# Kernel optimization log

Measured on AMD Instinct MI355X. Metric: run time of the kernel, lower is better.

Reference implementation:

```python
import math
import jax, jax.numpy as jnp
import numpy as np

B, S, D = 2, 2048, 512
H = 8
DH = D // H  # 64
FF = 2048


def _uniform(key, shape, c):
    return jax.random.uniform(key, shape, jnp.float32, -c, c)


def setup_inputs() -> dict:
    key = jax.random.key(0)
    ks = jax.random.split(key, 16)
    x = jax.random.normal(ks[0], (B, S, D), jnp.float32)
    c_qkv = math.sqrt(6 / (D + DH))
    wq = _uniform(ks[1], (H, D, DH), c_qkv)
    wk = _uniform(ks[2], (H, D, DH), c_qkv)
    wv = _uniform(ks[3], (H, D, DH), c_qkv)
    bq = jnp.zeros((H, DH), jnp.float32)
    bk = jnp.zeros((H, DH), jnp.float32)
    bv = jnp.zeros((H, DH), jnp.float32)
    c_o = math.sqrt(6 / (H * DH + D))
    wo = _uniform(ks[4], (H * DH, D), c_o)  # stored as (in, out)
    bo = jnp.zeros((D,), jnp.float32)
    gamma1 = jnp.ones((D,), jnp.float32)
    beta1 = jnp.zeros((D,), jnp.float32)
    c_ff = math.sqrt(6 / (D + FF))
    w1 = _uniform(ks[5], (D, FF), c_ff)
    b1 = jnp.zeros((FF,), jnp.float32)
    w2 = _uniform(ks[6], (FF, D), c_ff)
    b2 = jnp.zeros((D,), jnp.float32)
    gamma2 = jnp.ones((D,), jnp.float32)
    beta2 = jnp.zeros((D,), jnp.float32)
    return dict(x=x, wq=wq, bq=bq, wk=wk, bk=bk, wv=wv, bv=bv, wo=wo, bo=bo,
                gamma1=gamma1, beta1=beta1, w1=w1, b1=b1, w2=w2, b2=b2,
                gamma2=gamma2, beta2=beta2)


def _layernorm(x, gamma, beta):
    # matches torch: (x - mean) / std(unbiased=False), no epsilon in denom
    mean = jnp.mean(x, axis=-1, keepdims=True)
    var = jnp.mean((x - mean) ** 2, axis=-1, keepdims=True)
    return gamma * (x - mean) / jnp.sqrt(var) + beta


def reference(x, wq, bq, wk, bk, wv, bv, wo, bo, gamma1, beta1, w1, b1, w2, b2, gamma2, beta2):
    # multi-head attention: all heads batched in one einsum (same math as the per-head loop)
    q = jnp.einsum('bsd,hde->bhse', x, wq) + bq[None, :, None, :]
    k = jnp.einsum('bsd,hde->bhse', x, wk) + bk[None, :, None, :]
    v = jnp.einsum('bsd,hde->bhse', x, wv) + bv[None, :, None, :]
    scores = jnp.einsum('bhse,bhte->bhst', q, k) / math.sqrt(DH)  # [B,H,S,S]
    attn = jax.nn.softmax(scores, axis=-1)
    y = jnp.einsum('bhst,bhte->bhse', attn, v)  # [B,H,S,DH]
    y = y.transpose(0, 2, 1, 3).reshape(B, S, H * DH)
    y = y @ wo + bo
    # residual + LN (dropout is identity in eval)
    y = _layernorm(y + x, gamma1, beta1)
    # feedforward
    f = jax.nn.relu(y @ w1 + b1) @ w2 + b2
    out = _layernorm(f + y, gamma2, beta2)
    return out
```

## Files before the change

kernel.cpp:

```cpp
#include <hip/hip_runtime.h>

typedef __bf16 bf16;
typedef __attribute__((ext_vector_type(4))) __bf16 bf16x4;
typedef __attribute__((ext_vector_type(8))) __bf16 bf16x8;
typedef __attribute__((ext_vector_type(4))) float f32x4;
typedef __attribute__((ext_vector_type(16))) float f32x16;

#define DEV __device__ __forceinline__

DEV f32x4 mfma16(bf16x8 a, bf16x8 b, f32x4 c) {
  return __builtin_amdgcn_mfma_f32_16x16x32_bf16(a, b, c, 0, 0, 0);
}
DEV f32x16 mfma32(bf16x8 a, bf16x8 b, f32x16 c) {
  return __builtin_amdgcn_mfma_f32_32x32x16_bf16(a, b, c, 0, 0, 0);
}
DEV void gll16(const bf16* g, bf16* l) {
  __builtin_amdgcn_global_load_lds(
      (const __attribute__((address_space(1))) void*)g,
      (__attribute__((address_space(3))) void*)l, 16, 0, 0);
}
DEV unsigned cvtpk(float a, float b) {
  unsigned r;
  asm("v_cvt_pk_bf16_f32 %0, %1, %2" : "=v"(r) : "v"(a), "v"(b));
  return r;
}
DEV void pl32swap(unsigned& x, unsigned& y) {
  asm("v_permlane32_swap_b32 %0, %1" : "+v"(x), "+v"(y));
}

#define QSCALE 0.18033688f

__global__ __launch_bounds__(256) void prep_k(
    const float* __restrict__ x, const float* __restrict__ wq,
    const float* __restrict__ wk, const float* __restrict__ wv,
    const float* __restrict__ wo, const float* __restrict__ w1,
    const float* __restrict__ w2, const float* __restrict__ bq,
    const float* __restrict__ bk, const float* __restrict__ bv,
    bf16* __restrict__ xb, bf16* __restrict__ wqkvT, bf16* __restrict__ woT,
    bf16* __restrict__ w1T, bf16* __restrict__ w2T, float* __restrict__ cb) {
  const int blk = blockIdx.x, tid = threadIdx.x;
  if (blk < 1024) {
    int i = blk * 256 + tid;
    const float4* p = (const float4*)x + (size_t)i * 2;
    float4 a = p[0], b = p[1];
    bf16x8 o;
    o[0] = (bf16)a.x; o[1] = (bf16)a.y; o[2] = (bf16)a.z; o[3] = (bf16)a.w;
    o[4] = (bf16)b.x; o[5] = (bf16)b.y; o[6] = (bf16)b.z; o[7] = (bf16)b.w;
    ((bf16x8*)xb)[i] = o;
    return;
  }
  if (blk == 1792) {
    for (int i = tid; i < 1536; i += 256)
      cb[i] = i < 512 ? bq[i] : (i < 1024 ? bk[i - 512] : bv[i - 1024]);
    return;
  }
  __shared__ float tile[64][65];
  const int t = blk - 1024;
  const float* src;
  bf16* dst;
  int C, Rout, r0, c0;
  if (t < 192) {
    int mat = t / 64, rem = t % 64, head = rem >> 3, rt = rem & 7;
    src = (mat == 0 ? wq : mat == 1 ? wk : wv) + head * 32768;
    dst = wqkvT + (size_t)(mat * 8 + head) * 32768;
    C = 64; Rout = 512; r0 = rt * 64; c0 = 0;
  } else if (t < 256) {
    int t2 = t - 192;
    src = wo; dst = woT; C = 512; Rout = 512;
    r0 = (t2 >> 3) * 64; c0 = (t2 & 7) * 64;
  } else if (t < 512) {
    int t2 = t - 256;
    src = w1; dst = w1T; C = 2048; Rout = 512;
    r0 = (t2 >> 5) * 64; c0 = (t2 & 31) * 64;
  } else {
    int t2 = t - 512;
    src = w2; dst = w2T; C = 512; Rout = 2048;
    r0 = (t2 >> 3) * 64; c0 = (t2 & 7) * 64;
  }
#pragma unroll
  for (int j = 0; j < 4; ++j) {
    int e = j * 256 + tid;
    int r = e >> 4, c4 = e & 15;
    float4 f = *(const float4*)(src + (size_t)(r0 + r) * C + c0 + c4 * 4);
    tile[r][c4 * 4 + 0] = f.x;
    tile[r][c4 * 4 + 1] = f.y;
    tile[r][c4 * 4 + 2] = f.z;
    tile[r][c4 * 4 + 3] = f.w;
  }
  __syncthreads();
  const int co = tid >> 2, rr0 = (tid & 3) * 16;
  bf16x8 o0, o1;
#pragma unroll
  for (int k = 0; k < 8; ++k) o0[k] = (bf16)tile[rr0 + k][co];
#pragma unroll
  for (int k = 0; k < 8; ++k) o1[k] = (bf16)tile[rr0 + 8 + k][co];
  bf16* dp = dst + (size_t)(c0 + co) * Rout + r0 + rr0;
  *(bf16x8*)dp = o0;
  *(bf16x8*)(dp + 8) = o1;
}

template <int EPI>
__global__ __launch_bounds__(256) void gemmN64(
    const bf16* __restrict__ A, const bf16* __restrict__ Bt,
    const float* __restrict__ bias, float* __restrict__ outf,
    bf16* __restrict__ outb, bf16* __restrict__ vtb,
    int M, int N, int K, int klen) {
  __shared__ bf16 As[128 * 64];
  __shared__ bf16 Bs[64 * 64];
  const int tid = threadIdx.x;
  const int w = tid >> 6, l = tid & 63;
  const int lh = l & 15, lg = l >> 4;
  const int m0 = blockIdx.x * 128, n0 = blockIdx.y * 64;
  const int k0 = blockIdx.z * klen;
  const int mb = (w & 1) * 64, nb = (w >> 1) * 32;
  f32x4 acc[4][2] = {};
  for (int kt = k0; kt < k0 + klen; kt += 64) {
    __syncthreads();
#pragma unroll
    for (int j = 0; j < 4; ++j) {
      int slot = j * 256 + tid;
      int r = slot >> 3, cc = slot & 7;
      int kk = kt + ((cc ^ (r & 7)) << 3);
      gll16(A + (size_t)(m0 + r) * K + kk, As + slot * 8);
    }
#pragma unroll
    for (int j = 0; j < 2; ++j) {
      int slot = j * 256 + tid;
      int r = slot >> 3, cc = slot & 7;
      int kk = kt + ((cc ^ (r & 7)) << 3);
      gll16(Bt + (size_t)(n0 + r) * K + kk, Bs + slot * 8);
    }
    __syncthreads();
#pragma unroll
    for (int kk = 0; kk < 2; ++kk) {
      bf16x8 af[4], bfr[2];
#pragma unroll
      for (int mi = 0; mi < 4; ++mi) {
        int r = mb + mi * 16 + lh;
        af[mi] = *(const bf16x8*)(As + r * 64 + (((kk * 4 + lg) ^ (r & 7)) << 3));
      }
#pragma unroll
      for (int ni = 0; ni < 2; ++ni) {
        int r = nb + ni * 16 + lh;
        bfr[ni] = *(const bf16x8*)(Bs + r * 64 + (((kk * 4 + lg) ^ (r & 7)) << 3));
      }
#pragma unroll
      for (int mi = 0; mi < 4; ++mi)
#pragma unroll
        for (int ni = 0; ni < 2; ++ni)
          acc[mi][ni] = mfma16(af[mi], bfr[ni], acc[mi][ni]);
    }
  }
  float* op = (EPI == 0) ? outf + (size_t)blockIdx.z * M * N : nullptr;
#pragma unroll
  for (int mi = 0; mi < 4; ++mi)
#pragma unroll
    for (int ni = 0; ni < 2; ++ni) {
      const int row0 = m0 + mb + mi * 16 + lg * 4;
      const int col = n0 + nb + ni * 16 + lh;
      if (EPI == 2 && col >= 1024) {
        const int vcol = col - 1024;
        const int bhv = (row0 >> 11) * 8 + (vcol >> 6);
        const int dh = vcol & 63, s = row0 & 2047;
        bf16x4 q4;
#pragma unroll
        for (int i = 0; i < 4; ++i) q4[i] = (bf16)(acc[mi][ni][i] + bias[col]);
        *(bf16x4*)(vtb + (size_t)bhv * 131072 + (size_t)dh * 2048 + s) = q4;
        continue;
      }
#pragma unroll
      for (int i = 0; i < 4; ++i) {
        const int row = row0 + i;
        float v = acc[mi][ni][i];
        if (EPI == 0) {
          op[(size_t)row * N + col] = v;
        } else if (EPI == 1) {
          v += bias[col];
          outb[(size_t)row * N + col] = (bf16)fmaxf(v, 0.f);
        } else {
          v += bias[col];
          outb[(size_t)row * N + col] = (bf16)(col < 512 ? v * QSCALE : v);
        }
      }
    }
}

__global__ __launch_bounds__(512) void attn_fwd2(
    const bf16* __restrict__ qkv,
    const bf16* __restrict__ vtb,
    bf16* __restrict__ Y) {
  __shared__ __align__(16) char lds[65536];
  const int tid = threadIdx.x;
  const int w = tid >> 6, lane = tid & 63;
  const int l31 = lane & 31, h = lane >> 5;
  const int bh = blockIdx.y, b = bh >> 3, hh = bh & 7;
  const int qtile = blockIdx.x;
  const int half = w >> 2, wp = w & 3;
  const int q0 = qtile * 128 + wp * 32;
  const int tl = tid & 255, sh = tid >> 8;

  bf16x8 qf[4];
  {
    const size_t rowQ = (size_t)(b * 2048 + q0 + l31) * 1536 + hh * 64;
#pragma unroll
    for (int g = 0; g < 4; ++g)
      qf[g] = *(const bf16x8*)(qkv + rowQ + g * 16 + h * 8);
  }
  const bf16* Kp = qkv + 512 + hh * 64;
  const bf16* Vp = vtb + (size_t)bh * 131072;

  f32x16 oacc[2] = {};
  float m_run = -1e30f, l_run = 0.f;

#define KBUF(d, hf) ((bf16*)(lds + (d) * 32768 + (hf) * 16384))
#define VBUF(d, hf) ((bf16*)(lds + (d) * 32768 + (hf) * 16384 + 8192))

  auto stage = [&](int i, int d) {
    const int k0 = sh * 1024 + i * 64;
#pragma unroll
    for (int j = 0; j < 2; ++j) {
      int slot = j * 256 + tl;
      int r = slot >> 3, cc = slot & 7;
      gll16(Kp + (size_t)(b * 2048 + k0 + r) * 1536 + ((cc ^ (r & 7)) << 3),
            KBUF(d, sh) + slot * 8);
      gll16(Vp + (size_t)r * 2048 + k0 + ((cc ^ (r & 7)) << 3),
            VBUF(d, sh) + slot * 8);
    }
  };

  stage(0, 0);
  __syncthreads();
  for (int i = 0; i < 16; ++i) {
    const int d = i & 1;
    if (i < 15) stage(i + 1, d ^ 1);
    const bf16* Kt = KBUF(d, half);
    const bf16* Vt = VBUF(d, half);
    f32x16 st[2];
    __builtin_amdgcn_s_setprio(1);
#pragma unroll
    for (int kt = 0; kt < 2; ++kt) {
      f32x16 z = {};
      const int r = kt * 32 + l31;
#pragma unroll
      for (int g = 0; g < 4; ++g) {
        bf16x8 kf = *(const bf16x8*)(Kt + r * 64 + (((2 * g + h) ^ (r & 7)) << 3));
        z = mfma32(kf, qf[g], z);
      }
      st[kt] = z;
    }
    __builtin_amdgcn_s_setprio(0);
    float mx = -1e30f;
#pragma unroll
    for (int kt = 0; kt < 2; ++kt)
#pragma unroll
      for (int r = 0; r < 16; ++r) mx = fmaxf(mx, st[kt][r]);
    mx = fmaxf(mx, __shfl_xor(mx, 32, 64));
    if (!__all(mx <= m_run + 8.f)) {
      const float m_new = fmaxf(m_run, mx);
      const float scl = exp2f(m_run - m_new);
      l_run *= scl;
      oacc[0] = oacc[0] * scl;
      oacc[1] = oacc[1] * scl;
      m_run = m_new;
    }
    float ps = 0.f;
#pragma unroll
    for (int kt = 0; kt < 2; ++kt)
#pragma unroll
      for (int r = 0; r < 16; ++r) {
        const float e = exp2f(st[kt][r] - m_run);
        st[kt][r] = e;
        ps += e;
      }
    ps += __shfl_xor(ps, 32, 64);
    l_run += ps;
    bf16x8 pf[4];
#pragma unroll
    for (int kt = 0; kt < 2; ++kt)
#pragma unroll
      for (int g = 0; g < 2; ++g) {
        unsigned a0 = cvtpk(st[kt][8 * g + 0], st[kt][8 * g + 1]);
        unsigned a1 = cvtpk(st[kt][8 * g + 2], st[kt][8 * g + 3]);
        unsigned b0 = cvtpk(st[kt][8 * g + 4], st[kt][8 * g + 5]);
        unsigned b1 = cvtpk(st[kt][8 * g + 6], st[kt][8 * g + 7]);
        pl32swap(a0, b0);
        pl32swap(a1, b1);
        union { unsigned u[4]; bf16x8 v; } pk;
        pk.u[0] = a0; pk.u[1] = a1; pk.u[2] = b0; pk.u[3] = b1;
        pf[kt * 2 + g] = pk.v;
      }
    __builtin_amdgcn_s_setprio(1);
#pragma unroll
    for (int t = 0; t < 2; ++t) {
      const int r = t * 32 + l31;
#pragma unroll
      for (int kg = 0; kg < 4; ++kg) {
        bf16x8 vf = *(const bf16x8*)(Vt + r * 64 + (((2 * kg + h) ^ (r & 7)) << 3));
        oacc[t] = mfma32(vf, pf[kg], oacc[t]);
      }
    }
    __builtin_amdgcn_s_setprio(0);
    __syncthreads();
  }

  if (half == 1) {
    char* ob = lds + wp * 8192;
#pragma unroll
    for (int t = 0; t < 2; ++t)
#pragma unroll
      for (int c = 0; c < 4; ++c) {
        f32x4 v4 = {oacc[t][c * 4 + 0], oacc[t][c * 4 + 1],
                    oacc[t][c * 4 + 2], oacc[t][c * 4 + 3]};
        *(f32x4*)(ob + (t * 4 + c) * 1024 + lane * 16) = v4;
      }
    ((float2*)(lds + 32768))[wp * 64 + lane] = make_float2(m_run, l_run);
  }
  __syncthreads();
  bf16* Yt = (bf16*)(lds + 34816);
  if (half == 0) {
    float2 ml2 = ((const float2*)(lds + 32768))[wp * 64 + lane];
    const float mstar = fmaxf(m_run, ml2.x);
    const float e1 = exp2f(m_run - mstar), e2 = exp2f(ml2.x - mstar);
    const float lstar = l_run * e1 + ml2.y * e2;
    const float r1 = e1 / lstar, r2 = e2 / lstar;
    const char* ob = lds + wp * 8192;
#pragma unroll
    for (int t = 0; t < 2; ++t)
#pragma unroll
      for (int c = 0; c < 4; ++c) {
        f32x4 v4 = *(const f32x4*)(ob + (t * 4 + c) * 1024 + lane * 16);
#pragma unroll
        for (int j = 0; j < 4; ++j)
          oacc[t][c * 4 + j] = oacc[t][c * 4 + j] * r1 + v4[j] * r2;
      }
#pragma unroll
    for (int t = 0; t < 2; ++t)
#pragma unroll
      for (int r = 0; r < 16; ++r) {
        int dh = (r & 3) + 8 * (r >> 2) + 4 * h + 32 * t;
        Yt[(wp * 32 + l31) * 72 + dh] = (bf16)oacc[t][r];
      }
  }
  __syncthreads();
#pragma unroll
  for (int it = 0; it < 2; ++it) {
    int s = it * 512 + tid;
    int ql = s >> 3, cbk = s & 7;
    bf16x8 v = *(const bf16x8*)(Yt + ql * 72 + cbk * 8);
    *(bf16x8*)(Y + (size_t)(b * 2048 + qtile * 128 + ql) * 512 + hh * 64 + cbk * 8) = v;
  }
#undef KBUF
#undef VBUF
}

__global__ __launch_bounds__(256) void add_ln1_k(
    const float* __restrict__ P,
    const float* __restrict__ xres, const float* __restrict__ bias,
    const float* __restrict__ gamma, const float* __restrict__ beta,
    bf16* __restrict__ outb) {
  const int row = blockIdx.x, tid = threadIdx.x;
  const size_t base = (size_t)row * 512;
  const float2 p0 = ((const float2*)(P + base))[tid];
  const float2 p1 = ((const float2*)(P + 2097152 + base))[tid];
  const float2 xr = ((const float2*)(xres + base))[tid];
  const int c = tid * 2;
  float s0 = p0.x + p1.x + bias[c] + xr.x;
  float s1 = p0.y + p1.y + bias[c + 1] + xr.y;
  float sum = s0 + s1;
#pragma unroll
  for (int m = 1; m < 64; m <<= 1) sum += __shfl_xor(sum, m, 64);
  __shared__ float part[4], part2[4];
  const int w = tid >> 6, l = tid & 63;
  if (l == 0) part[w] = sum;
  __syncthreads();
  const float mean = (part[0] + part[1] + part[2] + part[3]) * (1.f / 512.f);
  const float d0 = s0 - mean, d1 = s1 - mean;
  float vs = d0 * d0 + d1 * d1;
#pragma unroll
  for (int m = 1; m < 64; m <<= 1) vs += __shfl_xor(vs, m, 64);
  if (l == 0) part2[w] = vs;
  __syncthreads();
  const float var = (part2[0] + part2[1] + part2[2] + part2[3]) * (1.f / 512.f);
  const float inv = rsqrtf(var);
  outb[base + c] = (bf16)(gamma[c] * (d0 * inv) + beta[c]);
  outb[base + c + 1] = (bf16)(gamma[c + 1] * (d1 * inv) + beta[c + 1]);
}

__global__ __launch_bounds__(256) void add_ln2_k(
    const float* __restrict__ P,
    const bf16* __restrict__ rres, const float* __restrict__ bias,
    const float* __restrict__ gamma, const float* __restrict__ beta,
    float* __restrict__ outf) {
  const int row = blockIdx.x, tid = threadIdx.x;
  const size_t base = (size_t)row * 512;
  const float2 p0 = ((const float2*)(P + base))[tid];
  const float2 p1 = ((const float2*)(P + 2097152 + base))[tid];
  const int c = tid * 2;
  float s0 = p0.x + p1.x + bias[c] + (float)rres[base + c];
  float s1 = p0.y + p1.y + bias[c + 1] + (float)rres[base + c + 1];
  float sum = s0 + s1;
#pragma unroll
  for (int m = 1; m < 64; m <<= 1) sum += __shfl_xor(sum, m, 64);
  __shared__ float part[4], part2[4];
  const int w = tid >> 6, l = tid & 63;
  if (l == 0) part[w] = sum;
  __syncthreads();
  const float mean = (part[0] + part[1] + part[2] + part[3]) * (1.f / 512.f);
  const float d0 = s0 - mean, d1 = s1 - mean;
  float vs = d0 * d0 + d1 * d1;
#pragma unroll
  for (int m = 1; m < 64; m <<= 1) vs += __shfl_xor(vs, m, 64);
  if (l == 0) part2[w] = vs;
  __syncthreads();
  const float var = (part2[0] + part2[1] + part2[2] + part2[3]) * (1.f / 512.f);
  const float inv = rsqrtf(var);
  ((float2*)(outf + base))[tid] =
      make_float2(gamma[c] * (d0 * inv) + beta[c], gamma[c + 1] * (d1 * inv) + beta[c + 1]);
}

extern "C" void kernel_launch(void* const* d_in, const int* in_sizes, int n_in,
                              void* d_out, int out_size, void* d_ws, size_t ws_size,
                              hipStream_t stream) {
  const float* x = (const float*)d_in[0];
  const float* wq = (const float*)d_in[1];
  const float* bq = (const float*)d_in[2];
  const float* wk = (const float*)d_in[3];
  const float* bk = (const float*)d_in[4];
  const float* wv = (const float*)d_in[5];
  const float* bv = (const float*)d_in[6];
  const float* wo = (const float*)d_in[7];
  const float* bo = (const float*)d_in[8];
  const float* g1 = (const float*)d_in[9];
  const float* be1 = (const float*)d_in[10];
  const float* w1 = (const float*)d_in[11];
  const float* b1 = (const float*)d_in[12];
  const float* w2 = (const float*)d_in[13];
  const float* b2 = (const float*)d_in[14];
  const float* g2 = (const float*)d_in[15];
  const float* be2 = (const float*)d_in[16];

  char* ws = (char*)d_ws;
  bf16* xb    = (bf16*)(ws + 0);
  bf16* y1b   = (bf16*)(ws + 0);
  bf16* wqkvT = (bf16*)(ws + 4194304);
  bf16* woT   = (bf16*)(ws + 5767168);
  bf16* w1T   = (bf16*)(ws + 6291456);
  bf16* w2T   = (bf16*)(ws + 8388608);
  float* cb   = (float*)(ws + 10485760);
  bf16* qkvb  = (bf16*)(ws + 10493952);
  float* t0   = (float*)(ws + 10493952);
  bf16* f1    = (bf16*)(ws + 10493952);
  bf16* vtb   = (bf16*)(ws + 23078656);
  bf16* yb    = (bf16*)(ws + 27272960);
  float* f2   = (float*)(ws + 27272960);

  prep_k<<<1793, 256, 0, stream>>>(x, wq, wk, wv, wo, w1, w2, bq, bk, bv,
                                   xb, wqkvT, woT, w1T, w2T, cb);

  gemmN64<2><<<dim3(32, 24, 1), 256, 0, stream>>>(xb, wqkvT, cb, nullptr, qkvb, vtb,
                                                  4096, 1536, 512, 512);
  attn_fwd2<<<dim3(16, 16), 512, 0, stream>>>(qkvb, vtb, yb);
  gemmN64<0><<<dim3(32, 8, 2), 256, 0, stream>>>(yb, woT, nullptr, t0, nullptr, nullptr,
                                                 4096, 512, 512, 256);
  add_ln1_k<<<4096, 256, 0, stream>>>(t0, x, bo, g1, be1, y1b);
  gemmN64<1><<<dim3(32, 32, 1), 256, 0, stream>>>(y1b, w1T, b1, nullptr, f1, nullptr,
                                                  4096, 2048, 512, 512);
  gemmN64<0><<<dim3(32, 8, 2), 256, 0, stream>>>(f1, w2T, nullptr, f2, nullptr, nullptr,
                                                 4096, 512, 2048, 1024);
  add_ln2_k<<<4096, 256, 0, stream>>>(f2, y1b, b2, g2, be2, (float*)d_out);
}
```

Baseline: 116.7 us.

## Shrink attention blocks to 64 queries and 32-key tiles for more blocks

The attention kernel now uses 256-thread blocks that each cover 64 query rows, so the grid grows from 256 to 512 workgroups. Each iteration stages a 32-key tile instead of 64, which needs a new V-transpose LDS layout and swizzle, and LDS use drops to about 42 KB. The aim is better occupancy and CU fill on a GPU with many compute units. In exchange, K/V are re-read from global memory by twice as many blocks, and the shorter per-iteration MFMA work means barriers and softmax bookkeeping weigh more.

```diff
diff --git a/kernel.cpp b/kernel.cpp
--- a/kernel.cpp
+++ b/kernel.cpp
@@ -185,19 +185,19 @@
     }
 }
 
-__global__ __launch_bounds__(512) void attn_fwd2(
+__global__ __launch_bounds__(256) void attn_fwd4(
     const bf16* __restrict__ qkv,
     const bf16* __restrict__ vtb,
     bf16* __restrict__ Y) {
-  __shared__ __align__(16) char lds[65536];
+  __shared__ __align__(16) char lds[43008];
   const int tid = threadIdx.x;
   const int w = tid >> 6, lane = tid & 63;
   const int l31 = lane & 31, h = lane >> 5;
   const int bh = blockIdx.y, b = bh >> 3, hh = bh & 7;
-  const int qtile = blockIdx.x;
-  const int half = w >> 2, wp = w & 3;
-  const int q0 = qtile * 128 + wp * 32;
-  const int tl = tid & 255, sh = tid >> 8;
+  const int qt = blockIdx.x;
+  const int wp = w & 1, half = w >> 1;
+  const int q0 = qt * 64 + wp * 32;
+  const int t128 = tid & 127, sh = tid >> 7;
 
   bf16x8 qf[4];
   {
@@ -212,48 +212,47 @@
   f32x16 oacc[2] = {};
   float m_run = -1e30f, l_run = 0.f;
 
-#define KBUF(d, hf) ((bf16*)(lds + (d) * 32768 + (hf) * 16384))
-#define VBUF(d, hf) ((bf16*)(lds + (d) * 32768 + (hf) * 16384 + 8192))
+#define KB4(d, hf) ((bf16*)(lds + (d) * 16384 + (hf) * 8192))
+#define VB4(d, hf) ((bf16*)(lds + (d) * 16384 + (hf) * 8192 + 4096))
 
   auto stage = [&](int i, int d) {
-    const int k0 = sh * 1024 + i * 64;
+    const int k0 = sh * 1024 + i * 32;
 #pragma unroll
     for (int j = 0; j < 2; ++j) {
-      int slot = j * 256 + tl;
-      int r = slot >> 3, cc = slot & 7;
-      gll16(Kp + (size_t)(b * 2048 + k0 + r) * 1536 + ((cc ^ (r & 7)) << 3),
-            KBUF(d, sh) + slot * 8);
-      gll16(Vp + (size_t)r * 2048 + k0 + ((cc ^ (r & 7)) << 3),
-            VBUF(d, sh) + slot * 8);
+      const int slot = j * 128 + t128;
+      const int kr = slot >> 3, kc = slot & 7;
+      gll16(Kp + (size_t)(b * 2048 + k0 + kr) * 1536 + ((kc ^ (kr & 7)) << 3),
+            KB4(d, sh) + slot * 8);
+      const int vp2 = slot >> 3, vc = slot & 7;
+      const int vsub = vc >> 2, vks = vc & 3;
+      gll16(Vp + (size_t)(2 * vp2 + vsub) * 2048 + k0 + ((vks ^ (vp2 & 3)) << 3),
+            VB4(d, sh) + slot * 8);
     }
   };
 
   stage(0, 0);
   __syncthreads();
-  for (int i = 0; i < 16; ++i) {
+  for (int i = 0; i < 32; ++i) {
     const int d = i & 1;
-    if (i < 15) stage(i + 1, d ^ 1);
-    const bf16* Kt = KBUF(d, half);
-    const bf16* Vt = VBUF(d, half);
-    f32x16 st[2];
+    if (i < 31) stage(i + 1, d ^ 1);
+    const bf16* Kt = KB4(d, half);
+    const bf16* Vt = VB4(d, half);
+    f32x16 st;
     __builtin_amdgcn_s_setprio(1);
-#pragma unroll
-    for (int kt = 0; kt < 2; ++kt) {
+    {
       f32x16 z = {};
-      const int r = kt * 32 + l31;
+      const int r = l31;
 #pragma unroll
       for (int g = 0; g < 4; ++g) {
         bf16x8 kf = *(const bf16x8*)(Kt + r * 64 + (((2 * g + h) ^ (r & 7)) << 3));
         z = mfma32(kf, qf[g], z);
       }
-      st[kt] = z;
+      st = z;
     }
     __builtin_amdgcn_s_setprio(0);
-    float mx = -1e30f;
-#pragma unroll
-    for (int kt = 0; kt < 2; ++kt)
-#pragma unroll
-      for (int r = 0; r < 16; ++r) mx = fmaxf(mx, st[kt][r]);
+    float mx = st[0];
+#pragma unroll
+    for (int r = 1; r < 16; ++r) mx = fmaxf(mx, st[r]);
     mx = fmaxf(mx, __shfl_xor(mx, 32, 64));
     if (!__all(mx <= m_run + 8.f)) {
       const float m_new = fmaxf(m_run, mx);
@@ -265,37 +264,35 @@
     }
     float ps = 0.f;
 #pragma unroll
-    for (int kt = 0; kt < 2; ++kt)
-#pragma unroll
-      for (int r = 0; r < 16; ++r) {
-        const float e = exp2f(st[kt][r] - m_run);
-        st[kt][r] = e;
-        ps += e;
-      }
+    for (int r = 0; r < 16; ++r) {
+      const float e = exp2f(st[r] - m_run);
+      st[r] = e;
+      ps += e;
+    }
     ps += __shfl_xor(ps, 32, 64);
     l_run += ps;
-    bf16x8 pf[4];
-#pragma unroll
-    for (int kt = 0; kt < 2; ++kt)
-#pragma unroll
-      for (int g = 0; g < 2; ++g) {
-        unsigned a0 = cvtpk(st[kt][8 * g + 0], st[kt][8 * g + 1]);
-        unsigned a1 = cvtpk(st[kt][8 * g + 2], st[kt][8 * g + 3]);
-        unsigned b0 = cvtpk(st[kt][8 * g + 4], st[kt][8 * g + 5]);
-        unsigned b1 = cvtpk(st[kt][8 * g + 6], st[kt][8 * g + 7]);
-        pl32swap(a0, b0);
-        pl32swap(a1, b1);
-        union { unsigned u[4]; bf16x8 v; } pk;
-        pk.u[0] = a0; pk.u[1] = a1; pk.u[2] = b0; pk.u[3] = b1;
-        pf[kt * 2 + g] = pk.v;
-      }
+    bf16x8 pf[2];
+#pragma unroll
+    for (int g = 0; g < 2; ++g) {
+      unsigned a0 = cvtpk(st[8 * g + 0], st[8 * g + 1]);
+      unsigned a1 = cvtpk(st[8 * g + 2], st[8 * g + 3]);
+      unsigned b0 = cvtpk(st[8 * g + 4], st[8 * g + 5]);
+      unsigned b1 = cvtpk(st[8 * g + 6], st[8 * g + 7]);
+      pl32swap(a0, b0);
+      pl32swap(a1, b1);
+      union { unsigned u[4]; bf16x8 v; } pk;
+      pk.u[0] = a0; pk.u[1] = a1; pk.u[2] = b0; pk.u[3] = b1;
+      pf[g] = pk.v;
+    }
     __builtin_amdgcn_s_setprio(1);
 #pragma unroll
     for (int t = 0; t < 2; ++t) {
-      const int r = t * 32 + l31;
-#pragma unroll
-      for (int kg = 0; kg < 4; ++kg) {
-        bf16x8 vf = *(const bf16x8*)(Vt + r * 64 + (((2 * kg + h) ^ (r & 7)) << 3));
+      const int dhr = t * 32 + l31;
+      const int rp = dhr >> 1, sb = dhr & 1;
+#pragma unroll
+      for (int kg = 0; kg < 2; ++kg) {
+        bf16x8 vf = *(const bf16x8*)(Vt + rp * 64 + sb * 32 +
+                                     (((2 * kg + h) ^ (rp & 3)) << 3));
         oacc[t] = mfma32(vf, pf[kg], oacc[t]);
       }
     }
@@ -316,7 +313,7 @@
     ((float2*)(lds + 32768))[wp * 64 + lane] = make_float2(m_run, l_run);
   }
   __syncthreads();
-  bf16* Yt = (bf16*)(lds + 34816);
+  bf16* Yt = (bf16*)(lds + 33792);
   if (half == 0) {
     float2 ml2 = ((const float2*)(lds + 32768))[wp * 64 + lane];
     const float mstar = fmaxf(m_run, ml2.x);
@@ -344,13 +341,13 @@
   __syncthreads();
 #pragma unroll
   for (int it = 0; it < 2; ++it) {
-    int s = it * 512 + tid;
+    int s = it * 256 + tid;
     int ql = s >> 3, cbk = s & 7;
     bf16x8 v = *(const bf16x8*)(Yt + ql * 72 + cbk * 8);
-    *(bf16x8*)(Y + (size_t)(b * 2048 + qtile * 128 + ql) * 512 + hh * 64 + cbk * 8) = v;
-  }
-#undef KBUF
-#undef VBUF
+    *(bf16x8*)(Y + (size_t)(b * 2048 + qt * 64 + ql) * 512 + hh * 64 + cbk * 8) = v;
+  }
+#undef KB4
+#undef VB4
 }
 
 __global__ __launch_bounds__(256) void add_ln1_k(
@@ -459,7 +456,7 @@
 
   gemmN64<2><<<dim3(32, 24, 1), 256, 0, stream>>>(xb, wqkvT, cb, nullptr, qkvb, vtb,
                                                   4096, 1536, 512, 512);
-  attn_fwd2<<<dim3(16, 16), 512, 0, stream>>>(qkvb, vtb, yb);
+  attn_fwd4<<<dim3(32, 16), 256, 0, stream>>>(qkvb, vtb, yb);
   gemmN64<0><<<dim3(32, 8, 2), 256, 0, stream>>>(yb, woT, nullptr, t0, nullptr, nullptr,
                                                  4096, 512, 512, 256);
   add_ln1_k<<<4096, 256, 0, stream>>>(t0, x, bo, g1, be1, y1b);
```

Measured after the change: 127.3 us. 9.1% more time.
